# Optimization experiments

Measured on AMD Instinct MI355X. Metric: run time of the kernel, lower is better.

The kernel has to match this reference:

```python
import jax, jax.numpy as jnp
import numpy as np

B, C, H, W = 4, 256, 64, 64
CP = C // 4  # embedding_channels, k=4 hardcoded
# branch index -> (key-stream i, query/value-stream j); streams: 0=t,1=b,2=m
IIDX = np.array([0, 0, 0, 1, 1, 1, 2, 2, 2])  # which stream feeds k
JIDX = np.array([0, 1, 2, 0, 1, 2, 0, 1, 2])  # which stream feeds q and v


def setup_inputs() -> dict:
    key = jax.random.key(0)
    ks = jax.random.split(key, 6)
    scale = 0.05
    return {
        "t": jax.random.normal(ks[0], (B, C, H, W), jnp.float32),
        "b": jax.random.normal(ks[1], (B, C, H, W), jnp.float32),
        "m": jax.random.normal(ks[2], (B, C, H, W), jnp.float32),
        "W_qkv": jax.random.normal(ks[3], (9, C, C), jnp.float32) * scale,
        "W_red": jax.random.normal(ks[4], (9, CP, C), jnp.float32) * scale,
        "W_rec": jax.random.normal(ks[5], (9, C, CP), jnp.float32) * scale,
    }


def _pool(x):
    # ChannelAttention: global avg pool + global max pool -> [B, C']
    return jnp.mean(x, axis=(2, 3)) + jnp.max(x, axis=(2, 3))


def _channel_attention(q, k, v, w_red, w_rec):
    # q,k,v: [B,C,H,W]; w_red: [C',C]; w_rec: [C,C']
    ori = q + k + v
    red = lambda x: jax.nn.relu(jnp.einsum("bchw,ec->behw", x, w_red))
    qr, kr, vr = red(q), red(k), red(v)
    f = _pool(kr)  # key   -> [B,C']
    g = _pool(qr)  # query -> [B,C']
    h = _pool(vr)  # value -> [B,C']
    # s = f^T g : [B,C',C']; softmax over dim=1 (rows), per torch nn.Softmax(dim=1)
    s = f[:, :, None] * g[:, None, :]
    beta = jax.nn.softmax(s, axis=1)
    vout = jnp.einsum("bi,bij->bj", h, beta)  # [B,C']
    # recovery 1x1 conv on [B,C',1,1]; bilinear upsample from 1x1 == broadcast
    o = jax.nn.sigmoid(jnp.einsum("be,ce->bc", vout, w_rec))  # [B,C]
    return o[:, :, None, None] * ori


def reference(t, b, m, W_qkv, W_red, W_rec):
    x = jnp.stack([t, b, m])  # [3,B,C,H,W]
    Wp = W_qkv.reshape(3, 3, C, C)  # [stream, (q,k,v), C_out, C_in]
    proj = jnp.einsum("sbchw,sjec->sjbehw", x, Wp)  # [3,3,B,C,H,W]
    Q, K, V = proj[:, 0], proj[:, 1], proj[:, 2]  # each [3,B,C,H,W]
    q9, k9, v9 = Q[JIDX], K[IIDX], V[JIDX]  # [9,B,C,H,W]
    outs = jax.vmap(_channel_attention)(q9, k9, v9, W_red, W_rec)
    return outs.sum(axis=0)
```

## Files before the change

### kernel.cpp

```cpp
#include <hip/hip_runtime.h>

#define Bn 4
#define Cn 256
#define HWn 4096
#define CPn 64
#define MP 640

typedef unsigned short u16;
typedef unsigned int u32;

using short8  = __attribute__((ext_vector_type(8))) short;
using floatx4 = __attribute__((ext_vector_type(4))) float;

static __device__ __forceinline__ u16 f2bf(float f) {
    union { float f; u32 u; } v; v.f = f;
    u32 r = (v.u + 0x7FFFu + ((v.u >> 16) & 1u)) >> 16;
    return (u16)r;
}

static __device__ __forceinline__ void gld16(const u16* g, u16* l) {
    __builtin_amdgcn_global_load_lds(
        (const __attribute__((address_space(1))) u32*)g,
        (__attribute__((address_space(3))) u32*)l, 16, 0, 0);
}

__global__ __launch_bounds__(256) void convert_transpose(
    const float* __restrict__ Tt, const float* __restrict__ Bt, const float* __restrict__ Mt,
    u16* __restrict__ xT)
{
    const int s  = blockIdx.z, b = blockIdx.y;
    const int ct = blockIdx.x & 3, hwt = blockIdx.x >> 2;
    const int c0 = ct * 64, hw0 = hwt * 64;
    const float* X = (s == 0 ? Tt : (s == 1 ? Bt : Mt)) + (size_t)b * Cn * HWn;

    __shared__ u16 T[64][72];
    const int t = threadIdx.x;
    const int cl = t >> 2, q = t & 3;

    const float* src = X + (size_t)(c0 + cl) * HWn + hw0 + q * 16;
    #pragma unroll
    for (int u = 0; u < 4; ++u) {
        const float4 v = *(const float4*)(src + u * 4);
        T[cl][q * 16 + u * 4 + 0] = f2bf(v.x);
        T[cl][q * 16 + u * 4 + 1] = f2bf(v.y);
        T[cl][q * 16 + u * 4 + 2] = f2bf(v.z);
        T[cl][q * 16 + u * 4 + 3] = f2bf(v.w);
    }
    __syncthreads();

    const int wl = t >> 2;
    u16* dst = xT + ((size_t)((s * Bn + b) * HWn) + hw0 + wl) * Cn + c0 + q * 16;
    #pragma unroll
    for (int u = 0; u < 2; ++u) {
        u32 w0 = (u32)T[q * 16 + u * 8 + 0][wl] | ((u32)T[q * 16 + u * 8 + 1][wl] << 16);
        u32 w1 = (u32)T[q * 16 + u * 8 + 2][wl] | ((u32)T[q * 16 + u * 8 + 3][wl] << 16);
        u32 w2 = (u32)T[q * 16 + u * 8 + 4][wl] | ((u32)T[q * 16 + u * 8 + 5][wl] << 16);
        u32 w3 = (u32)T[q * 16 + u * 8 + 6][wl] | ((u32)T[q * 16 + u * 8 + 7][wl] << 16);
        uint4 pk = {w0, w1, w2, w3};
        *(uint4*)(dst + u * 8) = pk;
    }
}

__global__ __launch_bounds__(256) void compose_red(
    const float* __restrict__ Wqkv, const float* __restrict__ Wred,
    u16* __restrict__ CWp)
{
    const int s  = blockIdx.z;
    const int tt = blockIdx.y / 3, m3 = blockIdx.y % 3;
    const int c0 = blockIdx.x * 64;
    const int idx = (tt == 1) ? (3 * s + m3) : (3 * m3 + s);

    const float* A = Wred + (size_t)idx * CPn * Cn;
    const float* Bm = Wqkv + (size_t)(3 * s + tt) * Cn * Cn;

    __shared__ float As[16][64];
    __shared__ float Bs[16][64];
    const int t = threadIdx.x;
    const int ty = t >> 4, tx = t & 15;
    float acc[4][4] = {};

    for (int k0 = 0; k0 < Cn; k0 += 16) {
        {
            const int r = t >> 2, eq = (t & 3) * 4;
            const float4 a = *(const float4*)(A + (size_t)r * Cn + k0 + eq);
            As[eq + 0][r] = a.x; As[eq + 1][r] = a.y; As[eq + 2][r] = a.z; As[eq + 3][r] = a.w;
        }
        {
            const int r = t >> 4, cq = (t & 15) * 4;
            *(float4*)(&Bs[r][cq]) = *(const float4*)(Bm + (size_t)(k0 + r) * Cn + c0 + cq);
        }
        __syncthreads();
        #pragma unroll
        for (int k = 0; k < 16; ++k) {
            const float4 a4 = *(const float4*)(&As[k][ty * 4]);
            const float4 b4 = *(const float4*)(&Bs[k][tx * 4]);
            const float a[4] = {a4.x, a4.y, a4.z, a4.w};
            const float bb[4] = {b4.x, b4.y, b4.z, b4.w};
            #pragma unroll
            for (int i = 0; i < 4; ++i)
                #pragma unroll
                for (int j = 0; j < 4; ++j)
                    acc[i][j] = fmaf(a[i], bb[j], acc[i][j]);
        }
        __syncthreads();
    }

    u16* out = CWp + (size_t)s * MP * Cn;
    #pragma unroll
    for (int i = 0; i < 4; ++i) {
        const int row = tt * 192 + m3 * 64 + ty * 4 + i;
        unsigned long long pk =
            (unsigned long long)f2bf(acc[i][0]) |
            ((unsigned long long)f2bf(acc[i][1]) << 16) |
            ((unsigned long long)f2bf(acc[i][2]) << 32) |
            ((unsigned long long)f2bf(acc[i][3]) << 48);
        *(unsigned long long*)(out + (size_t)row * Cn + c0 + tx * 4) = pk;
    }
}

__global__ __launch_bounds__(256) void redpool_mfma(
    const u16* __restrict__ xT, const u16* __restrict__ CWp,
    float* __restrict__ pool_sum, u32* __restrict__ pool_max)
{
    const int s  = blockIdx.z;
    const int mt = blockIdx.x >> 7, nt = blockIdx.x & 127;
    const int m0 = mt * 128, n0 = nt * 128;

    const u16* Ap = CWp + (size_t)s * MP * Cn;
    const u16* Bp = xT + (size_t)s * Bn * HWn * Cn;

    __shared__ __align__(16) u16 As[128 * 64];
    __shared__ __align__(16) u16 Bs[128 * 64];

    const int t = threadIdx.x;
    const int w = t >> 6, lane = t & 63;
    const int l15 = lane & 15, q = lane >> 4;
    const int srow = lane >> 3, scol = (lane & 7) * 8;
    const int rb = (w >> 1) * 64, cb = (w & 1) * 64;

    floatx4 acc[4][4] = {};

    for (int k0 = 0; k0 < Cn; k0 += 64) {
        #pragma unroll
        for (int i = 0; i < 4; ++i) {
            const int r = w * 32 + i * 8;
            gld16(Ap + (size_t)(m0 + r + srow) * Cn + k0 + scol, &As[r * 64]);
            gld16(Bp + (size_t)(n0 + r + srow) * Cn + k0 + scol, &Bs[r * 64]);
        }
        __syncthreads();
        #pragma unroll
        for (int kk = 0; kk < 2; ++kk) {
            const int ks = kk * 32 + q * 8;
            short8 af[4], bf[4];
            #pragma unroll
            for (int i = 0; i < 4; ++i) af[i] = *(const short8*)&As[(rb + i * 16 + l15) * 64 + ks];
            #pragma unroll
            for (int j = 0; j < 4; ++j) bf[j] = *(const short8*)&Bs[(cb + j * 16 + l15) * 64 + ks];
            #pragma unroll
            for (int i = 0; i < 4; ++i)
                #pragma unroll
                for (int j = 0; j < 4; ++j)
                    acc[i][j] = __builtin_amdgcn_mfma_f32_16x16x32_bf16(af[i], bf[j], acc[i][j], 0, 0, 0);
        }
        __syncthreads();
    }

    const int b = n0 >> 12;
    #pragma unroll
    for (int i = 0; i < 4; ++i) {
        #pragma unroll
        for (int r = 0; r < 4; ++r) {
            float rs = 0.f, rm = 0.f;
            #pragma unroll
            for (int j = 0; j < 4; ++j) {
                const float v = fmaxf(acc[i][j][r], 0.f);
                rs += v; rm = fmaxf(rm, v);
            }
            #pragma unroll
            for (int off = 1; off < 16; off <<= 1) {
                rs += __shfl_xor(rs, off);
                rm = fmaxf(rm, __shfl_xor(rm, off));
            }
            if (l15 == 0) {
                const int R = m0 + rb + i * 16 + q * 4 + r;
                if (R < 576) {
                    const int tt = R / 192, m3 = (R / 64) % 3, cp = R & 63;
                    const int idx = (tt == 1) ? (3 * s + m3) : (3 * m3 + s);
                    const int pidx = ((tt * 9 + idx) * Bn + b) * CPn + cp;
                    atomicAdd(&pool_sum[pidx], rs);
                    atomicMax(&pool_max[pidx], __float_as_uint(rm));
                }
            }
        }
    }
}

__global__ __launch_bounds__(256) void attn_small(
    const float* __restrict__ pool_sum, const u32* __restrict__ pool_max,
    const float* __restrict__ Wrec,
    float* __restrict__ coefA, float* __restrict__ coefK)
{
    const int idx = blockIdx.x / Bn;
    const int bb  = blockIdx.x % Bn;
    __shared__ float ff[CPn], gg[CPn], hh[CPn], vout[CPn];
    const int t = threadIdx.x;

    if (t < CPn) {
        int base;
        base = ((0 * 9 + idx) * Bn + bb) * CPn + t;
        gg[t] = pool_sum[base] * (1.0f / HWn) + __uint_as_float(pool_max[base]);
        base = ((1 * 9 + idx) * Bn + bb) * CPn + t;
        ff[t] = pool_sum[base] * (1.0f / HWn) + __uint_as_float(pool_max[base]);
        base = ((2 * 9 + idx) * Bn + bb) * CPn + t;
        hh[t] = pool_sum[base] * (1.0f / HWn) + __uint_as_float(pool_max[base]);
    }
    __syncthreads();

    if (t < CPn) {
        const float gj = gg[t];
        float mx = -1e30f;
        for (int i = 0; i < CPn; ++i) mx = fmaxf(mx, ff[i] * gj);
        float den = 0.f, num = 0.f;
        for (int i = 0; i < CPn; ++i) {
            const float e = expf(ff[i] * gj - mx);
            den += e;
            num += hh[i] * e;
        }
        vout[t] = num / den;
    }
    __syncthreads();

    {
        const float* wr = Wrec + ((size_t)idx * Cn + t) * CPn;
        float a = 0.f;
        for (int e = 0; e < CPn; ++e) a += vout[e] * wr[e];
        const float o = 1.0f / (1.0f + expf(-a));
        const int sj = idx % 3;
        const int si = idx / 3;
        atomicAdd(coefA + (sj * Bn + bb) * Cn + t, o);
        atomicAdd(coefK + (si * Bn + bb) * Cn + t, o);
    }
}

__global__ __launch_bounds__(256) void build_M(
    const float* __restrict__ Wqkv,
    const float* __restrict__ coefA, const float* __restrict__ coefK,
    u16* __restrict__ Mm)
{
    const int s = blockIdx.x >> 8, m = blockIdx.x & 255;
    const int b = blockIdx.y;
    const int t = threadIdx.x;
    const float cA = coefA[(s * Bn + b) * Cn + m];
    const float cK = coefK[(s * Bn + b) * Cn + m];
    const float wq = Wqkv[((size_t)(3 * s + 0) * Cn + m) * Cn + t];
    const float wk = Wqkv[((size_t)(3 * s + 1) * Cn + m) * Cn + t];
    const float wv = Wqkv[((size_t)(3 * s + 2) * Cn + m) * Cn + t];
    Mm[((size_t)(b * 256 + m)) * 768 + s * 256 + t] = f2bf(cA * (wq + wv) + cK * wk);
}

__global__ __launch_bounds__(256) void final_mfma(
    const u16* __restrict__ xT, const u16* __restrict__ Mm,
    float* __restrict__ out)
{
    const int b  = blockIdx.y;
    const int mt = blockIdx.x >> 6, nt = blockIdx.x & 63;
    const int m0 = mt * 128, n0 = nt * 64;

    __shared__ __align__(16) u16 As[128 * 64];
    __shared__ __align__(16) u16 Bs[64 * 64];

    const int t = threadIdx.x;
    const int w = t >> 6, lane = t & 63;
    const int l15 = lane & 15, q = lane >> 4;
    const int srow = lane >> 3, scol = (lane & 7) * 8;
    const int rb = (w >> 1) * 64, cb = (w & 1) * 32;

    const u16* Apb = Mm + (size_t)(b * 256 + m0) * 768;

    floatx4 acc[4][2] = {};

    for (int k0 = 0; k0 < 768; k0 += 64) {
        const int s = k0 >> 8, c0 = k0 & 255;
        const u16* Bpb = xT + ((size_t)((s * Bn + b) * HWn) + n0) * Cn + c0;
        #pragma unroll
        for (int i = 0; i < 4; ++i) {
            const int r = w * 32 + i * 8;
            gld16(Apb + (size_t)(r + srow) * 768 + k0 + scol, &As[r * 64]);
        }
        {
            const int r = w * 16 + 0;
            gld16(Bpb + (size_t)(r + srow) * Cn + scol, &Bs[r * 64]);
            const int r2 = w * 16 + 8;
            gld16(Bpb + (size_t)(r2 + srow) * Cn + scol, &Bs[r2 * 64]);
        }
        __syncthreads();
        #pragma unroll
        for (int kk = 0; kk < 2; ++kk) {
            const int ks = kk * 32 + q * 8;
            short8 af[4], bf[2];
            #pragma unroll
            for (int i = 0; i < 4; ++i) af[i] = *(const short8*)&As[(rb + i * 16 + l15) * 64 + ks];
            #pragma unroll
            for (int j = 0; j < 2; ++j) bf[j] = *(const short8*)&Bs[(cb + j * 16 + l15) * 64 + ks];
            #pragma unroll
            for (int i = 0; i < 4; ++i)
                #pragma unroll
                for (int j = 0; j < 2; ++j)
                    acc[i][j] = __builtin_amdgcn_mfma_f32_16x16x32_bf16(af[i], bf[j], acc[i][j], 0, 0, 0);
        }
        __syncthreads();
    }

    #pragma unroll
    for (int i = 0; i < 4; ++i)
        #pragma unroll
        for (int j = 0; j < 2; ++j)
            #pragma unroll
            for (int r = 0; r < 4; ++r) {
                const int row = m0 + rb + i * 16 + q * 4 + r;
                const int col = n0 + cb + j * 16 + l15;
                out[((size_t)(b * 256) + row) * HWn + col] = acc[i][j][r];
            }
}

extern "C" void kernel_launch(void* const* d_in, const int* in_sizes, int n_in,
                              void* d_out, int out_size, void* d_ws, size_t ws_size,
                              hipStream_t stream)
{
    const float* Tt   = (const float*)d_in[0];
    const float* Bt   = (const float*)d_in[1];
    const float* Mt   = (const float*)d_in[2];
    const float* Wqkv = (const float*)d_in[3];
    const float* Wred = (const float*)d_in[4];
    const float* Wrec = (const float*)d_in[5];
    float* out = (float*)d_out;

    unsigned char* p = (unsigned char*)d_ws;
    u16* xT = (u16*)p;            p += (size_t)3 * Bn * HWn * Cn * 2;
    u16* Mm = (u16*)p;            p += (size_t)Bn * 256 * 768 * 2;
    unsigned char* zbase = p;
    u16* CWp = (u16*)p;           p += (size_t)3 * MP * Cn * 2;
    float* pool_sum = (float*)p;  p += (size_t)27 * Bn * CPn * 4;
    u32*   pool_max = (u32*)p;    p += (size_t)27 * Bn * CPn * 4;
    float* coefA = (float*)p;     p += (size_t)3 * Bn * Cn * 4;
    float* coefK = (float*)p;     p += (size_t)3 * Bn * Cn * 4;
    const size_t zbytes = (size_t)(p - zbase);

    hipMemsetAsync(zbase, 0, zbytes, stream);

    compose_red      <<<dim3(4, 9, 3),    256, 0, stream>>>(Wqkv, Wred, CWp);
    convert_transpose<<<dim3(256, Bn, 3), 256, 0, stream>>>(Tt, Bt, Mt, xT);
    redpool_mfma     <<<dim3(640, 1, 3),  256, 0, stream>>>(xT, CWp, pool_sum, pool_max);
    attn_small       <<<9 * Bn,           256, 0, stream>>>(pool_sum, pool_max, Wrec, coefA, coefK);
    build_M          <<<dim3(768, Bn),    256, 0, stream>>>(Wqkv, coefA, coefK, Mm);
    final_mfma       <<<dim3(128, Bn),    256, 0, stream>>>(xT, Mm, out);
}
```

Before: 193.7 us.

## Enlarge MFMA tiles and store LDS operands in fragment-native layout

Both GEMM kernels, redpool_mfma and final_mfma, now use wider N tiles: 128x256 and 128x128. Shared memory is laid out in 16x32 fragment blocks so each lane reads its short8 operand contiguously (lane*8), which removes row-strided LDS reads and likely bank conflicts. The larger tiles raise the MFMA work per loaded byte and halve the grid sizes. In exchange, each kernel holds many more accumulator registers (launch_bounds 256,2) and launches fewer blocks, which may leave CUs underused.

```diff
diff --git a/kernel.cpp b/kernel.cpp
--- a/kernel.cpp
+++ b/kernel.cpp
@@ -23,6 +23,7 @@
         (const __attribute__((address_space(1))) u32*)g,
         (__attribute__((address_space(3))) u32*)l, 16, 0, 0);
 }
+
 
 __global__ __launch_bounds__(256) void convert_transpose(
     const float* __restrict__ Tt, const float* __restrict__ Bt, const float* __restrict__ Mt,
@@ -118,48 +119,54 @@
     }
 }
 
-__global__ __launch_bounds__(256) void redpool_mfma(
+__global__ __launch_bounds__(256, 2) void redpool_mfma(
     const u16* __restrict__ xT, const u16* __restrict__ CWp,
     float* __restrict__ pool_sum, u32* __restrict__ pool_max)
 {
     const int s  = blockIdx.z;
-    const int mt = blockIdx.x >> 7, nt = blockIdx.x & 127;
-    const int m0 = mt * 128, n0 = nt * 128;
+    const int mt = blockIdx.x >> 6, nt = blockIdx.x & 63;
+    const int m0 = mt * 128, n0 = nt * 256;
 
     const u16* Ap = CWp + (size_t)s * MP * Cn;
     const u16* Bp = xT + (size_t)s * Bn * HWn * Cn;
 
-    __shared__ __align__(16) u16 As[128 * 64];
-    __shared__ __align__(16) u16 Bs[128 * 64];
+    __shared__ __align__(16) u16 As[16 * 512];
+    __shared__ __align__(16) u16 Bs[32 * 512];
 
     const int t = threadIdx.x;
     const int w = t >> 6, lane = t & 63;
     const int l15 = lane & 15, q = lane >> 4;
-    const int srow = lane >> 3, scol = (lane & 7) * 8;
-    const int rb = (w >> 1) * 64, cb = (w & 1) * 64;
-
-    floatx4 acc[4][4] = {};
+    const int rb = (w >> 1) * 64, cb = (w & 1) * 128;
+
+    floatx4 acc[4][8] = {};
 
     for (int k0 = 0; k0 < Cn; k0 += 64) {
-        #pragma unroll
-        for (int i = 0; i < 4; ++i) {
-            const int r = w * 32 + i * 8;
-            gld16(Ap + (size_t)(m0 + r + srow) * Cn + k0 + scol, &As[r * 64]);
-            gld16(Bp + (size_t)(n0 + r + srow) * Cn + k0 + scol, &Bs[r * 64]);
+        const u16* Asrc = Ap + (size_t)m0 * Cn + k0 + (size_t)l15 * Cn + q * 8;
+        const u16* Bsrc = Bp + (size_t)n0 * Cn + k0 + (size_t)l15 * Cn + q * 8;
+        #pragma unroll
+        for (int pi = 0; pi < 4; ++pi) {
+            const int p = w * 4 + pi;
+            gld16(Asrc + (size_t)((p >> 1) * 16) * Cn + (p & 1) * 32, &As[p * 512]);
+        }
+        #pragma unroll
+        for (int pi = 0; pi < 8; ++pi) {
+            const int p = w * 8 + pi;
+            gld16(Bsrc + (size_t)((p >> 1) * 16) * Cn + (p & 1) * 32, &Bs[p * 512]);
         }
         __syncthreads();
         #pragma unroll
         for (int kk = 0; kk < 2; ++kk) {
-            const int ks = kk * 32 + q * 8;
-            short8 af[4], bf[4];
-            #pragma unroll
-            for (int i = 0; i < 4; ++i) af[i] = *(const short8*)&As[(rb + i * 16 + l15) * 64 + ks];
-            #pragma unroll
-            for (int j = 0; j < 4; ++j) bf[j] = *(const short8*)&Bs[(cb + j * 16 + l15) * 64 + ks];
+            short8 af[4], bf[8];
+            #pragma unroll
+            for (int i = 0; i < 4; ++i)
+                af[i] = *(const short8*)&As[((((w >> 1) * 4 + i) << 1) + kk) * 512 + lane * 8];
+            #pragma unroll
+            for (int j = 0; j < 8; ++j)
+                bf[j] = *(const short8*)&Bs[((((w & 1) * 8 + j) << 1) + kk) * 512 + lane * 8];
             #pragma unroll
             for (int i = 0; i < 4; ++i)
                 #pragma unroll
-                for (int j = 0; j < 4; ++j)
+                for (int j = 0; j < 8; ++j)
                     acc[i][j] = __builtin_amdgcn_mfma_f32_16x16x32_bf16(af[i], bf[j], acc[i][j], 0, 0, 0);
         }
         __syncthreads();
@@ -172,7 +179,7 @@
         for (int r = 0; r < 4; ++r) {
             float rs = 0.f, rm = 0.f;
             #pragma unroll
-            for (int j = 0; j < 4; ++j) {
+            for (int j = 0; j < 8; ++j) {
                 const float v = fmaxf(acc[i][j][r], 0.f);
                 rs += v; rm = fmaxf(rm, v);
             }
@@ -258,54 +265,50 @@
     Mm[((size_t)(b * 256 + m)) * 768 + s * 256 + t] = f2bf(cA * (wq + wv) + cK * wk);
 }
 
-__global__ __launch_bounds__(256) void final_mfma(
+__global__ __launch_bounds__(256, 2) void final_mfma(
     const u16* __restrict__ xT, const u16* __restrict__ Mm,
     float* __restrict__ out)
 {
     const int b  = blockIdx.y;
-    const int mt = blockIdx.x >> 6, nt = blockIdx.x & 63;
-    const int m0 = mt * 128, n0 = nt * 64;
-
-    __shared__ __align__(16) u16 As[128 * 64];
-    __shared__ __align__(16) u16 Bs[64 * 64];
+    const int mt = blockIdx.x >> 5, nt = blockIdx.x & 31;
+    const int m0 = mt * 128, n0 = nt * 128;
+
+    __shared__ __align__(16) u16 As[16 * 512];
+    __shared__ __align__(16) u16 Bs[16 * 512];
 
     const int t = threadIdx.x;
     const int w = t >> 6, lane = t & 63;
     const int l15 = lane & 15, q = lane >> 4;
-    const int srow = lane >> 3, scol = (lane & 7) * 8;
-    const int rb = (w >> 1) * 64, cb = (w & 1) * 32;
+    const int rb = (w >> 1) * 64, cb = (w & 1) * 64;
 
     const u16* Apb = Mm + (size_t)(b * 256 + m0) * 768;
 
-    floatx4 acc[4][2] = {};
+    floatx4 acc[4][4] = {};
 
     for (int k0 = 0; k0 < 768; k0 += 64) {
         const int s = k0 >> 8, c0 = k0 & 255;
-        const u16* Bpb = xT + ((size_t)((s * Bn + b) * HWn) + n0) * Cn + c0;
-        #pragma unroll
-        for (int i = 0; i < 4; ++i) {
-            const int r = w * 32 + i * 8;
-            gld16(Apb + (size_t)(r + srow) * 768 + k0 + scol, &As[r * 64]);
-        }
-        {
-            const int r = w * 16 + 0;
-            gld16(Bpb + (size_t)(r + srow) * Cn + scol, &Bs[r * 64]);
-            const int r2 = w * 16 + 8;
-            gld16(Bpb + (size_t)(r2 + srow) * Cn + scol, &Bs[r2 * 64]);
+        const u16* Asrc = Apb + k0 + (size_t)l15 * 768 + q * 8;
+        const u16* Bsrc = xT + ((size_t)((s * Bn + b) * HWn) + n0 + l15) * Cn + c0 + q * 8;
+        #pragma unroll
+        for (int pi = 0; pi < 4; ++pi) {
+            const int p = w * 4 + pi;
+            gld16(Asrc + (size_t)((p >> 1) * 16) * 768 + (p & 1) * 32, &As[p * 512]);
+            gld16(Bsrc + (size_t)((p >> 1) * 16) * Cn + (p & 1) * 32, &Bs[p * 512]);
         }
         __syncthreads();
         #pragma unroll
         for (int kk = 0; kk < 2; ++kk) {
-            const int ks = kk * 32 + q * 8;
-            short8 af[4], bf[2];
-            #pragma unroll
-            for (int i = 0; i < 4; ++i) af[i] = *(const short8*)&As[(rb + i * 16 + l15) * 64 + ks];
-            #pragma unroll
-            for (int j = 0; j < 2; ++j) bf[j] = *(const short8*)&Bs[(cb + j * 16 + l15) * 64 + ks];
+            short8 af[4], bf[4];
+            #pragma unroll
+            for (int i = 0; i < 4; ++i)
+                af[i] = *(const short8*)&As[((((w >> 1) * 4 + i) << 1) + kk) * 512 + lane * 8];
+            #pragma unroll
+            for (int j = 0; j < 4; ++j)
+                bf[j] = *(const short8*)&Bs[((((w & 1) * 4 + j) << 1) + kk) * 512 + lane * 8];
             #pragma unroll
             for (int i = 0; i < 4; ++i)
                 #pragma unroll
-                for (int j = 0; j < 2; ++j)
+                for (int j = 0; j < 4; ++j)
                     acc[i][j] = __builtin_amdgcn_mfma_f32_16x16x32_bf16(af[i], bf[j], acc[i][j], 0, 0, 0);
         }
         __syncthreads();
@@ -314,7 +317,7 @@
     #pragma unroll
     for (int i = 0; i < 4; ++i)
         #pragma unroll
-        for (int j = 0; j < 2; ++j)
+        for (int j = 0; j < 4; ++j)
             #pragma unroll
             for (int r = 0; r < 4; ++r) {
                 const int row = m0 + rb + i * 16 + q * 4 + r;
@@ -350,8 +353,8 @@
 
     compose_red      <<<dim3(4, 9, 3),    256, 0, stream>>>(Wqkv, Wred, CWp);
     convert_transpose<<<dim3(256, Bn, 3), 256, 0, stream>>>(Tt, Bt, Mt, xT);
-    redpool_mfma     <<<dim3(640, 1, 3),  256, 0, stream>>>(xT, CWp, pool_sum, pool_max);
+    redpool_mfma     <<<dim3(320, 1, 3),  256, 0, stream>>>(xT, CWp, pool_sum, pool_max);
     attn_small       <<<9 * Bn,           256, 0, stream>>>(pool_sum, pool_max, Wrec, coefA, coefK);
     build_M          <<<dim3(768, Bn),    256, 0, stream>>>(Wqkv, coefA, coefK, Mm);
-    final_mfma       <<<dim3(128, Bn),    256, 0, stream>>>(xT, Mm, out);
-}
+    final_mfma       <<<dim3(64, Bn),     256, 0, stream>>>(xT, Mm, out);
+}
```

Measured after the change: 188.4 us. 2.8% less time.
